# Optimization experiments

Hardware: AMD Instinct MI355X
Metric: run time of the kernel (lower is better)

## Reference

```python
import jax, jax.numpy as jnp
import numpy as np

N_NODES = 100000
N_EDGES = 3200000
IN_CH = 64
HID = [64, 32, 16]


def setup_inputs() -> dict:
    key = jax.random.key(0)
    ks = jax.random.split(key, 12)
    x = jax.random.normal(ks[0], (N_NODES, IN_CH), dtype=jnp.float32)
    edge_index = jax.random.randint(ks[1], (2, N_EDGES), 0, N_NODES, dtype=jnp.int32)
    dims = [IN_CH] + HID
    params = {}
    i = 2
    for l in range(3):
        din, dout = dims[l], dims[l + 1]
        sc = 1.0 / np.sqrt(din)
        params[f"Wl{l}"] = jax.random.uniform(ks[i], (din, dout), jnp.float32, -sc, sc); i += 1
        params[f"Wr{l}"] = jax.random.uniform(ks[i], (din, dout), jnp.float32, -sc, sc); i += 1
        params[f"b{l}"] = jnp.zeros((dout,), jnp.float32)
    sc = 1.0 / np.sqrt(HID[-1])
    params["Wc"] = jax.random.uniform(ks[i], (HID[-1], 1), jnp.float32, -sc, sc)
    params["bc"] = jnp.zeros((1,), jnp.float32)
    return dict(x=x, edge_index=edge_index, **params)


def _sage_conv(x, src, dst, Wl, Wr, b):
    # message = x[src]; mean-aggregate at dst; out = agg @ Wl + x @ Wr + b
    msg = x[src]  # [E, din]
    s = jax.ops.segment_sum(msg, dst, num_segments=N_NODES)
    cnt = jax.ops.segment_sum(jnp.ones((dst.shape[0],), x.dtype), dst, num_segments=N_NODES)
    agg = s / jnp.maximum(cnt, 1.0)[:, None]
    return agg @ Wl + x @ Wr + b


def reference(x, edge_index, Wl0, Wr0, b0, Wl1, Wr1, b1, Wl2, Wr2, b2, Wc, bc):
    src, dst = edge_index[0], edge_index[1]
    h = jax.nn.relu(_sage_conv(x, src, dst, Wl0, Wr0, b0))
    h = jax.nn.relu(_sage_conv(h, src, dst, Wl1, Wr1, b1))
    h = jax.nn.relu(_sage_conv(h, src, dst, Wl2, Wr2, b2))
    return h @ Wc + bc  # [N_NODES, 1]
```

## Files before the change

### kernel.cpp

```cpp
#include <hip/hip_runtime.h>


#define NN 100000
#define BSH 6
#define NBK ((NN + 63) >> 6)
#define HB 128
#define SRCMASK 0x1FFFF
#define NSEG 8192
#define SCB 32

__device__ __forceinline__ unsigned f2bf(float f) {
    unsigned u = __float_as_uint(f);
    u += 0x7fffu + ((u >> 16) & 1u);
    return u >> 16;
}
__device__ __forceinline__ float bflo(unsigned u) { return __uint_as_float(u << 16); }
__device__ __forceinline__ float bfhi(unsigned u) { return __uint_as_float(u & 0xffff0000u); }

__global__ void hist_k(const int* __restrict__ dst, int E, int* __restrict__ gh) {
    __shared__ int lh[NBK];
    for (int i = threadIdx.x; i < NBK; i += blockDim.x) lh[i] = 0;
    __syncthreads();
    int c = blockIdx.x;
    int chunk = (E + HB - 1) / HB;
    int b0 = c * chunk, e0 = min(b0 + chunk, E);
    for (int e = b0 + threadIdx.x; e < e0; e += blockDim.x)
        atomicAdd(&lh[dst[e] >> BSH], 1);
    __syncthreads();
    for (int i = threadIdx.x; i < NBK; i += blockDim.x) gh[i * HB + c] = lh[i];
}

__global__ void scanA_k(const int* __restrict__ gh, int M, int* __restrict__ segsum) {
    int t = blockIdx.x * blockDim.x + threadIdx.x;
    int cht = (M + NSEG - 1) / NSEG;
    int b0 = t * cht, e0 = min(b0 + cht, M);
    int s = 0;
    for (int i = b0; i < e0; ++i) s += gh[i];
    segsum[t] = s;
}

__global__ void scanB_k(int* __restrict__ segsum, int* __restrict__ gh, int M, int E) {
    __shared__ int part[1024];
    int tid = threadIdx.x;
    constexpr int SPT = NSEG / 1024;
    int loc[SPT];
    int s = 0;
#pragma unroll
    for (int k = 0; k < SPT; ++k) { loc[k] = segsum[tid * SPT + k]; s += loc[k]; }
    part[tid] = s;
    __syncthreads();
    for (int d = 1; d < 1024; d <<= 1) {
        int t = (tid >= d) ? part[tid - d] : 0;
        __syncthreads();
        part[tid] += t;
        __syncthreads();
    }
    int run = (tid == 0) ? 0 : part[tid - 1];
#pragma unroll
    for (int k = 0; k < SPT; ++k) { int t = loc[k]; segsum[tid * SPT + k] = run; run += t; }
    if (tid == 0) gh[M] = E;
}

__global__ void scanC_k(int* __restrict__ gh, int M, const int* __restrict__ segsum) {
    int t = blockIdx.x * blockDim.x + threadIdx.x;
    int cht = (M + NSEG - 1) / NSEG;
    int b0 = t * cht, e0 = min(b0 + cht, M);
    int run = segsum[t];
    for (int i = b0; i < e0; ++i) {
        int v = gh[i];
        gh[i] = run;
        run += v;
    }
}

__global__ void scatter_pack_k(const int* __restrict__ src, const int* __restrict__ dst,
                               int E, const int* __restrict__ gh,
                               unsigned* __restrict__ pair) {
    __shared__ int cur[NBK];
    int c = blockIdx.x;
    for (int i = threadIdx.x; i < NBK; i += blockDim.x) cur[i] = gh[i * HB + c];
    __syncthreads();
    int chunk = (E + HB - 1) / HB;
    int b0 = c * chunk, e0 = min(b0 + chunk, E);
    for (int e = b0 + threadIdx.x; e < e0; e += blockDim.x) {
        int dv = dst[e], sv = src[e];
        int p = atomicAdd(&cur[dv >> BSH], 1);
        pair[p] = (unsigned)sv | ((unsigned)(dv & 63) << 17);
    }
}

__global__ void sort_bucket_k(const unsigned* __restrict__ pair, const int* __restrict__ gh,
                              int* __restrict__ adj, int* __restrict__ off,
                              float* __restrict__ inv, int N, int E) {
    __shared__ int lcnt[64];
    __shared__ int lbase[64];
    int b = blockIdx.x, tid = threadIdx.x;
    int base = gh[b * HB], endp = gh[(b + 1) * HB];
    int v0 = b << BSH;
    int nv = min(64, N - v0);
    if (tid < 64) lcnt[tid] = 0;
    __syncthreads();
    for (int i = base + tid; i < endp; i += blockDim.x)
        atomicAdd(&lcnt[pair[i] >> 17], 1);
    __syncthreads();
    if (tid == 0) {
        int run = 0;
        for (int d = 0; d < 64; ++d) { lbase[d] = run; run += lcnt[d]; }
    }
    __syncthreads();
    if (tid < nv) {
        off[v0 + tid] = base + lbase[tid];
        inv[v0 + tid] = 1.0f / (float)max(lcnt[tid], 1);
    }
    if (b == NBK - 1 && tid == 0) off[N] = E;
    if (tid < 64) lcnt[tid] = lbase[tid];
    __syncthreads();
    for (int i = base + tid; i < endp; i += blockDim.x) {
        unsigned u = pair[i];
        int dl = u >> 17;
        int p = base + atomicAdd(&lcnt[dl], 1);
        adj[p] = u & SRCMASK;
    }
}

template <int DIN, int DOUT>
__global__ void transform2_k(const float* __restrict__ h,
                             const float* __restrict__ Wl, const float* __restrict__ Wr,
                             const float* __restrict__ bias,
                             unsigned* __restrict__ g, float2* __restrict__ r, int N) {
    constexpr int JP = DOUT / 2;
    __shared__ float2 sWl[DIN * JP];
    __shared__ float2 sWr[DIN * JP];
    __shared__ float2 sb[JP];
    const float2* Wl2 = (const float2*)Wl;
    const float2* Wr2 = (const float2*)Wr;
    for (int i = threadIdx.x; i < DIN * JP; i += blockDim.x) { sWl[i] = Wl2[i]; sWr[i] = Wr2[i]; }
    if (threadIdx.x < JP) sb[threadIdx.x] = ((const float2*)bias)[threadIdx.x];
    __syncthreads();
    int idx = blockIdx.x * blockDim.x + threadIdx.x;
    int NP = N / 2;
    if (idx >= NP * JP) return;
    int p = idx / JP, jp = idx % JP;
    int v0 = 2 * p, v1 = v0 + 1;
    const float* h0 = h + (size_t)v0 * DIN;
    const float* h1 = h + (size_t)v1 * DIN;
    float gl0x = 0, gl0y = 0, gl1x = 0, gl1y = 0;
    float gr0x = 0, gr0y = 0, gr1x = 0, gr1y = 0;
#pragma unroll
    for (int k = 0; k < DIN; ++k) {
        float2 wl = sWl[k * JP + jp];
        float2 wr = sWr[k * JP + jp];
        float a0 = h0[k], a1 = h1[k];
        gl0x = fmaf(a0, wl.x, gl0x); gl0y = fmaf(a0, wl.y, gl0y);
        gl1x = fmaf(a1, wl.x, gl1x); gl1y = fmaf(a1, wl.y, gl1y);
        gr0x = fmaf(a0, wr.x, gr0x); gr0y = fmaf(a0, wr.y, gr0y);
        gr1x = fmaf(a1, wr.x, gr1x); gr1y = fmaf(a1, wr.y, gr1y);
    }
    float2 bb = sb[jp];
    g[(size_t)v0 * JP + jp] = f2bf(gl0x) | (f2bf(gl0y) << 16);
    g[(size_t)v1 * JP + jp] = f2bf(gl1x) | (f2bf(gl1y) << 16);
    r[(size_t)v0 * JP + jp] = make_float2(gr0x + bb.x, gr0y + bb.y);
    r[(size_t)v1 * JP + jp] = make_float2(gr1x + bb.x, gr1y + bb.y);
}

template <int DOUT, int WAVES, int HEAD>
__global__ void agg_k(const unsigned* __restrict__ g, const int* __restrict__ off,
                      const int* __restrict__ adj, const float* __restrict__ invc,
                      const float* r, const float* __restrict__ Wc,
                      const float* __restrict__ bc, float* out, int N) {
    constexpr int Q8 = DOUT / 8;
    constexpr int EPT = 64 / Q8;
    __shared__ float sagg[WAVES][DOUT];
    int wid = threadIdx.x >> 6, lane = threadIdx.x & 63;
    int v = blockIdx.x * WAVES + wid;
    bool active = v < N;
    int q = lane & (Q8 - 1);
    int eg = lane / Q8;
    float acc[8] = {0, 0, 0, 0, 0, 0, 0, 0};
#define ACCU(U) do { \
        acc[0] += bflo(U.x); acc[1] += bfhi(U.x); \
        acc[2] += bflo(U.y); acc[3] += bfhi(U.y); \
        acc[4] += bflo(U.z); acc[5] += bfhi(U.z); \
        acc[6] += bflo(U.w); acc[7] += bfhi(U.w); } while (0)
    if (active) {
        int beg = off[v], end = off[v + 1];
        const uint4* g4 = (const uint4*)g;
        int i = beg + eg;
        for (; i + 3 * EPT < end; i += 4 * EPT) {
            int s0 = adj[i], s1 = adj[i + EPT], s2 = adj[i + 2 * EPT], s3 = adj[i + 3 * EPT];
            uint4 u0 = g4[(size_t)s0 * Q8 + q];
            uint4 u1 = g4[(size_t)s1 * Q8 + q];
            uint4 u2 = g4[(size_t)s2 * Q8 + q];
            uint4 u3 = g4[(size_t)s3 * Q8 + q];
            ACCU(u0); ACCU(u1); ACCU(u2); ACCU(u3);
        }
        for (; i < end; i += EPT) {
            int sv = adj[i];
            uint4 u = g4[(size_t)sv * Q8 + q];
            ACCU(u);
        }
#pragma unroll
        for (int d = Q8; d < 64; d <<= 1)
#pragma unroll
            for (int c = 0; c < 8; ++c) acc[c] += __shfl_xor(acc[c], d, 64);
        if (eg == 0) {
            float4* sp = (float4*)&sagg[wid][q * 8];
            sp[0] = make_float4(acc[0], acc[1], acc[2], acc[3]);
            sp[1] = make_float4(acc[4], acc[5], acc[6], acc[7]);
        }
    }
#undef ACCU
    __syncthreads();
    if (active && lane < DOUT) {
        float iv = invc[v];
        float val = fmaxf(fmaf(sagg[wid][lane], iv, r[(size_t)v * DOUT + lane]), 0.f);
        if (!HEAD) {
            out[(size_t)v * DOUT + lane] = val;
        } else {
            float pp = val * Wc[lane];
#pragma unroll
            for (int d = 1; d < 16; d <<= 1) pp += __shfl_xor(pp, d, 64);
            if (lane == 0) out[v] = pp + bc[0];
        }
    }
}

extern "C" void kernel_launch(void* const* d_in, const int* in_sizes, int n_in,
                              void* d_out, int out_size, void* d_ws, size_t ws_size,
                              hipStream_t stream) {
    const float* x   = (const float*)d_in[0];
    const int*   ei  = (const int*)d_in[1];
    const float* Wl0 = (const float*)d_in[2];
    const float* Wr0 = (const float*)d_in[3];
    const float* b0  = (const float*)d_in[4];
    const float* Wl1 = (const float*)d_in[5];
    const float* Wr1 = (const float*)d_in[6];
    const float* b1  = (const float*)d_in[7];
    const float* Wl2 = (const float*)d_in[8];
    const float* Wr2 = (const float*)d_in[9];
    const float* b2  = (const float*)d_in[10];
    const float* Wc  = (const float*)d_in[11];
    const float* bc  = (const float*)d_in[12];
    float* out = (float*)d_out;

    const int N = NN;
    const int E = in_sizes[1] / 2;
    const int* src = ei;
    const int* dst = ei + E;
    const int M = NBK * HB;

    char* ws = (char*)d_ws;
    const size_t KB = 1 << 10;
    const size_t MB = 1 << 20;
    int*      gh   = (int*)(ws + 0);
    int*      off  = (int*)(ws + 1 * MB);
    float*    inv  = (float*)(ws + 1536 * KB);
    int*      segs = (int*)(ws + 1950 * KB);
    unsigned* pair = (unsigned*)(ws + 2 * MB);
    int*      adj  = (int*)(ws + 15 * MB);
    unsigned* g0 = (unsigned*)(ws + 54 * MB);
    float*    r0 = (float*)(ws + 28 * MB);
    float*    h1 = r0;
    unsigned* g1 = (unsigned*)(ws + 2 * MB);
    float*    r1 = (float*)(ws + 54 * MB);
    float*    h2 = r1;
    unsigned* g2 = (unsigned*)(ws + 9 * MB);
    float*    r2 = (float*)(ws + 28 * MB);

    hist_k<<<HB, 256, 0, stream>>>(dst, E, gh);
    scanA_k<<<SCB, 256, 0, stream>>>(gh, M, segs);
    scanB_k<<<1, 1024, 0, stream>>>(segs, gh, M, E);
    scanC_k<<<SCB, 256, 0, stream>>>(gh, M, segs);
    scatter_pack_k<<<HB, 256, 0, stream>>>(src, dst, E, gh, pair);
    sort_bucket_k<<<NBK, 256, 0, stream>>>(pair, gh, adj, off, inv, N, E);

    transform2_k<64, 64><<<(N / 2 * 32 + 255) / 256, 256, 0, stream>>>(x, Wl0, Wr0, b0, g0, (float2*)r0, N);
    agg_k<64, 4, 0><<<(N + 3) / 4, 256, 0, stream>>>(g0, off, adj, inv, r0, nullptr, nullptr, h1, N);

    transform2_k<64, 32><<<(N / 2 * 16 + 255) / 256, 256, 0, stream>>>(h1, Wl1, Wr1, b1, g1, (float2*)r1, N);
    agg_k<32, 4, 0><<<(N + 3) / 4, 256, 0, stream>>>(g1, off, adj, inv, r1, nullptr, nullptr, h2, N);

    transform2_k<32, 16><<<(N / 2 * 8 + 255) / 256, 256, 0, stream>>>(h2, Wl2, Wr2, b2, g2, (float2*)r2, N);
    agg_k<16, 4, 1><<<(N + 3) / 4, 256, 0, stream>>>(g2, off, adj, inv, r2, Wc, bc, out, N);
}
```

Baseline: 442.2 us.

## Fuse histogram and local scatter into one pass, resolve bucket ranges per chunk

Replaces the separate histogram and global scatter kernels with a single kernel in which each of 256 chunks builds its local bucket histogram, does an in-block exclusive scan and scatters edges into its own contiguous region, keeping writes local to the chunk. A transpose kernel then reshapes the per-chunk counts and offsets so the global scan can run over them. The bucket sort kernel now reads each chunk's sub-range serially per thread instead of a single contiguous range. This removes the separate scatter pass over the edge list and its scattered global writes, but each sort thread now walks its segment serially and the bucket kernel's reads are split into many small pieces.

```diff
diff --git a/kernel.cpp b/kernel.cpp
--- a/kernel.cpp
+++ b/kernel.cpp
@@ -4,7 +4,7 @@
 #define NN 100000
 #define BSH 6
 #define NBK ((NN + 63) >> 6)
-#define HB 128
+#define HB 256
 #define SRCMASK 0x1FFFF
 #define NSEG 8192
 #define SCB 32
@@ -17,17 +17,74 @@
 __device__ __forceinline__ float bflo(unsigned u) { return __uint_as_float(u << 16); }
 __device__ __forceinline__ float bfhi(unsigned u) { return __uint_as_float(u & 0xffff0000u); }
 
-__global__ void hist_k(const int* __restrict__ dst, int E, int* __restrict__ gh) {
+__global__ void part1_k(const int* __restrict__ src, const int* __restrict__ dst,
+                        int E, int* __restrict__ ghT, int* __restrict__ gh2T,
+                        unsigned* __restrict__ pair) {
     __shared__ int lh[NBK];
-    for (int i = threadIdx.x; i < NBK; i += blockDim.x) lh[i] = 0;
-    __syncthreads();
-    int c = blockIdx.x;
+    __shared__ int part[512];
+    int c = blockIdx.x, tid = threadIdx.x;
     int chunk = (E + HB - 1) / HB;
     int b0 = c * chunk, e0 = min(b0 + chunk, E);
-    for (int e = b0 + threadIdx.x; e < e0; e += blockDim.x)
-        atomicAdd(&lh[dst[e] >> BSH], 1);
-    __syncthreads();
-    for (int i = threadIdx.x; i < NBK; i += blockDim.x) gh[i * HB + c] = lh[i];
+    for (int i = tid; i < NBK; i += 512) lh[i] = 0;
+    __syncthreads();
+    for (int e = b0 + tid; e < e0; e += 512) atomicAdd(&lh[dst[e] >> BSH], 1);
+    __syncthreads();
+    constexpr int CPT = (NBK + 511) / 512;
+    int myb = tid * CPT;
+    int s = 0;
+#pragma unroll
+    for (int k = 0; k < CPT; ++k) { int i = myb + k; if (i < NBK) s += lh[i]; }
+    part[tid] = s;
+    __syncthreads();
+    for (int d = 1; d < 512; d <<= 1) {
+        int t = (tid >= d) ? part[tid - d] : 0;
+        __syncthreads();
+        part[tid] += t;
+        __syncthreads();
+    }
+    int run = (tid == 0) ? 0 : part[tid - 1];
+#pragma unroll
+    for (int k = 0; k < CPT; ++k) {
+        int i = myb + k;
+        if (i < NBK) {
+            int cc = lh[i];
+            ghT[(size_t)c * NBK + i] = cc;
+            gh2T[(size_t)c * NBK + i] = run;
+            lh[i] = run;
+            run += cc;
+        }
+    }
+    __syncthreads();
+    for (int e = b0 + tid; e < e0; e += 512) {
+        int dv = dst[e], sv = src[e];
+        int p = b0 + atomicAdd(&lh[dv >> BSH], 1);
+        pair[p] = (unsigned)sv | ((unsigned)(dv & 63) << 17);
+    }
+}
+
+__global__ void transpose_k(const int* __restrict__ a, const int* __restrict__ b,
+                            int* __restrict__ at, int* __restrict__ bt) {
+    __shared__ int ta[32][33], tb[32][33];
+    int ib = blockIdx.x * 32;
+    int cb = blockIdx.y * 32;
+    int tx = threadIdx.x & 31, ty = threadIdx.x >> 5;
+#pragma unroll
+    for (int k = 0; k < 32; k += 8) {
+        int c = cb + ty + k, i = ib + tx;
+        if (c < HB && i < NBK) {
+            ta[ty + k][tx] = a[(size_t)c * NBK + i];
+            tb[ty + k][tx] = b[(size_t)c * NBK + i];
+        }
+    }
+    __syncthreads();
+#pragma unroll
+    for (int k = 0; k < 32; k += 8) {
+        int i = ib + ty + k, c = cb + tx;
+        if (i < NBK && c < HB) {
+            at[(size_t)i * HB + c] = ta[tx][ty + k];
+            bt[(size_t)i * HB + c] = tb[tx][ty + k];
+        }
+    }
 }
 
 __global__ void scanA_k(const int* __restrict__ gh, int M, int* __restrict__ segsum) {
@@ -39,7 +96,7 @@
     segsum[t] = s;
 }
 
-__global__ void scanB_k(int* __restrict__ segsum, int* __restrict__ gh, int M, int E) {
+__global__ void scanB_k(int* __restrict__ segsum) {
     __shared__ int part[1024];
     int tid = threadIdx.x;
     constexpr int SPT = NSEG / 1024;
@@ -58,7 +115,6 @@
     int run = (tid == 0) ? 0 : part[tid - 1];
 #pragma unroll
     for (int k = 0; k < SPT; ++k) { int t = loc[k]; segsum[tid * SPT + k] = run; run += t; }
-    if (tid == 0) gh[M] = E;
 }
 
 __global__ void scanC_k(int* __restrict__ gh, int M, const int* __restrict__ segsum) {
@@ -73,35 +129,24 @@
     }
 }
 
-__global__ void scatter_pack_k(const int* __restrict__ src, const int* __restrict__ dst,
-                               int E, const int* __restrict__ gh,
-                               unsigned* __restrict__ pair) {
-    __shared__ int cur[NBK];
-    int c = blockIdx.x;
-    for (int i = threadIdx.x; i < NBK; i += blockDim.x) cur[i] = gh[i * HB + c];
-    __syncthreads();
-    int chunk = (E + HB - 1) / HB;
-    int b0 = c * chunk, e0 = min(b0 + chunk, E);
-    for (int e = b0 + threadIdx.x; e < e0; e += blockDim.x) {
-        int dv = dst[e], sv = src[e];
-        int p = atomicAdd(&cur[dv >> BSH], 1);
-        pair[p] = (unsigned)sv | ((unsigned)(dv & 63) << 17);
-    }
-}
-
-__global__ void sort_bucket_k(const unsigned* __restrict__ pair, const int* __restrict__ gh,
+__global__ void sort_bucket_k(const unsigned* __restrict__ pair,
+                              const int* __restrict__ ghm, const int* __restrict__ gh2m,
                               int* __restrict__ adj, int* __restrict__ off,
                               float* __restrict__ inv, int N, int E) {
     __shared__ int lcnt[64];
     __shared__ int lbase[64];
     int b = blockIdx.x, tid = threadIdx.x;
-    int base = gh[b * HB], endp = gh[(b + 1) * HB];
+    int base = ghm[b * HB];
     int v0 = b << BSH;
     int nv = min(64, N - v0);
     if (tid < 64) lcnt[tid] = 0;
     __syncthreads();
-    for (int i = base + tid; i < endp; i += blockDim.x)
-        atomicAdd(&lcnt[pair[i] >> 17], 1);
+    int chunk = (E + HB - 1) / HB;
+    int c = tid;
+    int b0c = c * chunk, e0c = min(b0c + chunk, E);
+    int ls = b0c + gh2m[b * HB + c];
+    int le = (b == NBK - 1) ? e0c : (b0c + gh2m[(b + 1) * HB + c]);
+    for (int i = ls; i < le; ++i) atomicAdd(&lcnt[pair[i] >> 17], 1);
     __syncthreads();
     if (tid == 0) {
         int run = 0;
@@ -115,10 +160,9 @@
     if (b == NBK - 1 && tid == 0) off[N] = E;
     if (tid < 64) lcnt[tid] = lbase[tid];
     __syncthreads();
-    for (int i = base + tid; i < endp; i += blockDim.x) {
+    for (int i = ls; i < le; ++i) {
         unsigned u = pair[i];
-        int dl = u >> 17;
-        int p = base + atomicAdd(&lcnt[dl], 1);
+        int p = base + atomicAdd(&lcnt[u >> 17], 1);
         adj[p] = u & SRCMASK;
     }
 }
@@ -252,27 +296,30 @@
     char* ws = (char*)d_ws;
     const size_t KB = 1 << 10;
     const size_t MB = 1 << 20;
-    int*      gh   = (int*)(ws + 0);
-    int*      off  = (int*)(ws + 1 * MB);
-    float*    inv  = (float*)(ws + 1536 * KB);
-    int*      segs = (int*)(ws + 1950 * KB);
-    unsigned* pair = (unsigned*)(ws + 2 * MB);
-    int*      adj  = (int*)(ws + 15 * MB);
-    unsigned* g0 = (unsigned*)(ws + 54 * MB);
-    float*    r0 = (float*)(ws + 28 * MB);
+    int*      ghT  = (int*)(ws + 0);
+    int*      gh2T = (int*)(ws + 2 * MB);
+    int*      ghm  = (int*)(ws + 4 * MB);
+    int*      gh2m = (int*)(ws + 6 * MB);
+    int*      off  = (int*)(ws + 8 * MB);
+    float*    inv  = (float*)(ws + 8 * MB + 512 * KB);
+    int*      segs = (int*)(ws + 9 * MB);
+    unsigned* pair = (unsigned*)(ws + 10 * MB);
+    int*      adj  = (int*)(ws + 23 * MB);
+    unsigned* g0 = (unsigned*)(ws + 36 * MB);
+    float*    r0 = (float*)(ws + 49 * MB);
     float*    h1 = r0;
-    unsigned* g1 = (unsigned*)(ws + 2 * MB);
-    float*    r1 = (float*)(ws + 54 * MB);
+    unsigned* g1 = (unsigned*)(ws + 10 * MB);
+    float*    r1 = (float*)(ws + 36 * MB);
     float*    h2 = r1;
-    unsigned* g2 = (unsigned*)(ws + 9 * MB);
-    float*    r2 = (float*)(ws + 28 * MB);
-
-    hist_k<<<HB, 256, 0, stream>>>(dst, E, gh);
-    scanA_k<<<SCB, 256, 0, stream>>>(gh, M, segs);
-    scanB_k<<<1, 1024, 0, stream>>>(segs, gh, M, E);
-    scanC_k<<<SCB, 256, 0, stream>>>(gh, M, segs);
-    scatter_pack_k<<<HB, 256, 0, stream>>>(src, dst, E, gh, pair);
-    sort_bucket_k<<<NBK, 256, 0, stream>>>(pair, gh, adj, off, inv, N, E);
+    unsigned* g2 = (unsigned*)(ws + 17 * MB);
+    float*    r2 = (float*)(ws + 10 * MB);
+
+    part1_k<<<HB, 512, 0, stream>>>(src, dst, E, ghT, gh2T, pair);
+    transpose_k<<<dim3((NBK + 31) / 32, HB / 32), 256, 0, stream>>>(ghT, gh2T, ghm, gh2m);
+    scanA_k<<<SCB, 256, 0, stream>>>(ghm, M, segs);
+    scanB_k<<<1, 1024, 0, stream>>>(segs);
+    scanC_k<<<SCB, 256, 0, stream>>>(ghm, M, segs);
+    sort_bucket_k<<<NBK, HB, 0, stream>>>(pair, ghm, gh2m, adj, off, inv, N, E);
 
     transform2_k<64, 64><<<(N / 2 * 32 + 255) / 256, 256, 0, stream>>>(x, Wl0, Wr0, b0, g0, (float2*)r0, N);
     agg_k<64, 4, 0><<<(N + 3) / 4, 256, 0, stream>>>(g0, off, adj, inv, r0, nullptr, nullptr, h1, N);
```

Result: slower. 491.5 us (+11.2%).

## Restructure CSR build into three-kernel local-partition and bucket sort

Applied to the files above, without the earlier changes.

Replaces the six-kernel CSR construction (histogram, three-pass scan, scatter, per-64-node bucket sort) with three kernels. Each of 256 chunks histograms its edges into 196 coarse buckets of 512 nodes and scatters them locally within the chunk. A single block computes the bucket bases, and one block per bucket then gathers its slices from every chunk to produce the final adjacency lists, offsets and inverse degrees. This cuts launches and global scan passes, but the final sort walks each chunk slice serially per thread and runs only 196 blocks of 256 threads, which may underuse the GPU.

```diff
diff --git a/kernel.cpp b/kernel.cpp
--- a/kernel.cpp
+++ b/kernel.cpp
@@ -2,12 +2,11 @@
 
 
 #define NN 100000
-#define BSH 6
-#define NBK ((NN + 63) >> 6)
-#define HB 128
+#define BSH 9
+#define NBK ((NN + 511) >> 9)
+#define HB 256
 #define SRCMASK 0x1FFFF
-#define NSEG 8192
-#define SCB 32
+#define DLSH 17
 
 __device__ __forceinline__ unsigned f2bf(float f) {
     unsigned u = __float_as_uint(f);
@@ -17,108 +16,97 @@
 __device__ __forceinline__ float bflo(unsigned u) { return __uint_as_float(u << 16); }
 __device__ __forceinline__ float bfhi(unsigned u) { return __uint_as_float(u & 0xffff0000u); }
 
-__global__ void hist_k(const int* __restrict__ dst, int E, int* __restrict__ gh) {
+__global__ void part1_k(const int* __restrict__ src, const int* __restrict__ dst,
+                        int E, int* __restrict__ gcnt, int* __restrict__ goff,
+                        unsigned* __restrict__ pair) {
     __shared__ int lh[NBK];
-    for (int i = threadIdx.x; i < NBK; i += blockDim.x) lh[i] = 0;
-    __syncthreads();
-    int c = blockIdx.x;
+    __shared__ int part[512];
+    int c = blockIdx.x, tid = threadIdx.x;
     int chunk = (E + HB - 1) / HB;
     int b0 = c * chunk, e0 = min(b0 + chunk, E);
-    for (int e = b0 + threadIdx.x; e < e0; e += blockDim.x)
-        atomicAdd(&lh[dst[e] >> BSH], 1);
-    __syncthreads();
-    for (int i = threadIdx.x; i < NBK; i += blockDim.x) gh[i * HB + c] = lh[i];
-}
-
-__global__ void scanA_k(const int* __restrict__ gh, int M, int* __restrict__ segsum) {
-    int t = blockIdx.x * blockDim.x + threadIdx.x;
-    int cht = (M + NSEG - 1) / NSEG;
-    int b0 = t * cht, e0 = min(b0 + cht, M);
+    if (tid < NBK) lh[tid] = 0;
+    __syncthreads();
+    for (int e = b0 + tid; e < e0; e += 512) atomicAdd(&lh[dst[e] >> BSH], 1);
+    __syncthreads();
+    int cnt = (tid < NBK) ? lh[tid] : 0;
+    part[tid] = cnt;
+    __syncthreads();
+    for (int d = 1; d < 512; d <<= 1) {
+        int t = (tid >= d) ? part[tid - d] : 0;
+        __syncthreads();
+        part[tid] += t;
+        __syncthreads();
+    }
+    int run = (tid == 0) ? 0 : part[tid - 1];
+    if (tid < NBK) {
+        gcnt[(size_t)c * NBK + tid] = cnt;
+        goff[(size_t)c * NBK + tid] = run;
+        lh[tid] = run;
+    }
+    __syncthreads();
+    for (int e = b0 + tid; e < e0; e += 512) {
+        int dv = dst[e], sv = src[e];
+        int p = b0 + atomicAdd(&lh[dv >> BSH], 1);
+        pair[p] = (unsigned)sv | ((unsigned)(dv & 511) << DLSH);
+    }
+}
+
+__global__ void bsum_k(const int* __restrict__ gcnt, int* __restrict__ bb, int E) {
+    __shared__ int part[256];
+    int tid = threadIdx.x;
     int s = 0;
-    for (int i = b0; i < e0; ++i) s += gh[i];
-    segsum[t] = s;
-}
-
-__global__ void scanB_k(int* __restrict__ segsum, int* __restrict__ gh, int M, int E) {
-    __shared__ int part[1024];
-    int tid = threadIdx.x;
-    constexpr int SPT = NSEG / 1024;
-    int loc[SPT];
-    int s = 0;
-#pragma unroll
-    for (int k = 0; k < SPT; ++k) { loc[k] = segsum[tid * SPT + k]; s += loc[k]; }
+    if (tid < NBK)
+        for (int c = 0; c < HB; ++c) s += gcnt[(size_t)c * NBK + tid];
     part[tid] = s;
     __syncthreads();
-    for (int d = 1; d < 1024; d <<= 1) {
+    for (int d = 1; d < 256; d <<= 1) {
         int t = (tid >= d) ? part[tid - d] : 0;
         __syncthreads();
         part[tid] += t;
         __syncthreads();
     }
+    if (tid < NBK) bb[tid] = part[tid] - s;
+    if (tid == 0) bb[NBK] = E;
+}
+
+__global__ void sort2_k(const unsigned* __restrict__ pair, const int* __restrict__ goff,
+                        const int* __restrict__ bb, int* __restrict__ adj,
+                        int* __restrict__ off, float* __restrict__ inv, int N, int E) {
+    __shared__ int sls[HB], sle[HB];
+    __shared__ int lcnt[512], lcur[512];
+    __shared__ int part[256];
+    int b = blockIdx.x, tid = threadIdx.x;
+    int chunk = (E + HB - 1) / HB;
+    int b0c = tid * chunk, e0c = min(b0c + chunk, E);
+    sls[tid] = b0c + goff[(size_t)tid * NBK + b];
+    sle[tid] = (b + 1 < NBK) ? (b0c + goff[(size_t)tid * NBK + b + 1]) : e0c;
+    lcnt[tid] = 0; lcnt[tid + 256] = 0;
+    __syncthreads();
+    for (int i = sls[tid]; i < sle[tid]; ++i)
+        atomicAdd(&lcnt[pair[i] >> DLSH], 1);
+    __syncthreads();
+    int c0 = lcnt[2 * tid], c1 = lcnt[2 * tid + 1];
+    part[tid] = c0 + c1;
+    __syncthreads();
+    for (int d = 1; d < 256; d <<= 1) {
+        int t = (tid >= d) ? part[tid - d] : 0;
+        __syncthreads();
+        part[tid] += t;
+        __syncthreads();
+    }
     int run = (tid == 0) ? 0 : part[tid - 1];
-#pragma unroll
-    for (int k = 0; k < SPT; ++k) { int t = loc[k]; segsum[tid * SPT + k] = run; run += t; }
-    if (tid == 0) gh[M] = E;
-}
-
-__global__ void scanC_k(int* __restrict__ gh, int M, const int* __restrict__ segsum) {
-    int t = blockIdx.x * blockDim.x + threadIdx.x;
-    int cht = (M + NSEG - 1) / NSEG;
-    int b0 = t * cht, e0 = min(b0 + cht, M);
-    int run = segsum[t];
-    for (int i = b0; i < e0; ++i) {
-        int v = gh[i];
-        gh[i] = run;
-        run += v;
-    }
-}
-
-__global__ void scatter_pack_k(const int* __restrict__ src, const int* __restrict__ dst,
-                               int E, const int* __restrict__ gh,
-                               unsigned* __restrict__ pair) {
-    __shared__ int cur[NBK];
-    int c = blockIdx.x;
-    for (int i = threadIdx.x; i < NBK; i += blockDim.x) cur[i] = gh[i * HB + c];
-    __syncthreads();
-    int chunk = (E + HB - 1) / HB;
-    int b0 = c * chunk, e0 = min(b0 + chunk, E);
-    for (int e = b0 + threadIdx.x; e < e0; e += blockDim.x) {
-        int dv = dst[e], sv = src[e];
-        int p = atomicAdd(&cur[dv >> BSH], 1);
-        pair[p] = (unsigned)sv | ((unsigned)(dv & 63) << 17);
-    }
-}
-
-__global__ void sort_bucket_k(const unsigned* __restrict__ pair, const int* __restrict__ gh,
-                              int* __restrict__ adj, int* __restrict__ off,
-                              float* __restrict__ inv, int N, int E) {
-    __shared__ int lcnt[64];
-    __shared__ int lbase[64];
-    int b = blockIdx.x, tid = threadIdx.x;
-    int base = gh[b * HB], endp = gh[(b + 1) * HB];
+    int base = bb[b];
     int v0 = b << BSH;
-    int nv = min(64, N - v0);
-    if (tid < 64) lcnt[tid] = 0;
-    __syncthreads();
-    for (int i = base + tid; i < endp; i += blockDim.x)
-        atomicAdd(&lcnt[pair[i] >> 17], 1);
-    __syncthreads();
-    if (tid == 0) {
-        int run = 0;
-        for (int d = 0; d < 64; ++d) { lbase[d] = run; run += lcnt[d]; }
-    }
-    __syncthreads();
-    if (tid < nv) {
-        off[v0 + tid] = base + lbase[tid];
-        inv[v0 + tid] = 1.0f / (float)max(lcnt[tid], 1);
-    }
+    int vg0 = v0 + 2 * tid, vg1 = v0 + 2 * tid + 1;
+    if (vg0 < N) { off[vg0] = base + run;      inv[vg0] = 1.f / (float)max(c0, 1); }
+    if (vg1 < N) { off[vg1] = base + run + c0; inv[vg1] = 1.f / (float)max(c1, 1); }
+    lcur[2 * tid] = base + run;
+    lcur[2 * tid + 1] = base + run + c0;
     if (b == NBK - 1 && tid == 0) off[N] = E;
-    if (tid < 64) lcnt[tid] = lbase[tid];
-    __syncthreads();
-    for (int i = base + tid; i < endp; i += blockDim.x) {
+    __syncthreads();
+    for (int i = sls[tid]; i < sle[tid]; ++i) {
         unsigned u = pair[i];
-        int dl = u >> 17;
-        int p = base + atomicAdd(&lcnt[dl], 1);
+        int p = atomicAdd(&lcur[u >> DLSH], 1);
         adj[p] = u & SRCMASK;
     }
 }
@@ -247,32 +235,28 @@
     const int E = in_sizes[1] / 2;
     const int* src = ei;
     const int* dst = ei + E;
-    const int M = NBK * HB;
 
     char* ws = (char*)d_ws;
-    const size_t KB = 1 << 10;
     const size_t MB = 1 << 20;
-    int*      gh   = (int*)(ws + 0);
-    int*      off  = (int*)(ws + 1 * MB);
-    float*    inv  = (float*)(ws + 1536 * KB);
-    int*      segs = (int*)(ws + 1950 * KB);
-    unsigned* pair = (unsigned*)(ws + 2 * MB);
-    int*      adj  = (int*)(ws + 15 * MB);
-    unsigned* g0 = (unsigned*)(ws + 54 * MB);
-    float*    r0 = (float*)(ws + 28 * MB);
+    int*      gcnt = (int*)(ws + 0);
+    int*      goff = (int*)(ws + 1 * MB);
+    int*      bb   = (int*)(ws + 2 * MB);
+    int*      off  = (int*)(ws + 3 * MB);
+    float*    inv  = (float*)(ws + 3 * MB + 512 * 1024);
+    unsigned* pair = (unsigned*)(ws + 4 * MB);
+    int*      adj  = (int*)(ws + 17 * MB);
+    unsigned* g0 = (unsigned*)(ws + 30 * MB);
+    float*    r0 = (float*)(ws + 43 * MB);
     float*    h1 = r0;
-    unsigned* g1 = (unsigned*)(ws + 2 * MB);
-    float*    r1 = (float*)(ws + 54 * MB);
+    unsigned* g1 = (unsigned*)(ws + 4 * MB);
+    float*    r1 = (float*)(ws + 30 * MB);
     float*    h2 = r1;
-    unsigned* g2 = (unsigned*)(ws + 9 * MB);
-    float*    r2 = (float*)(ws + 28 * MB);
-
-    hist_k<<<HB, 256, 0, stream>>>(dst, E, gh);
-    scanA_k<<<SCB, 256, 0, stream>>>(gh, M, segs);
-    scanB_k<<<1, 1024, 0, stream>>>(segs, gh, M, E);
-    scanC_k<<<SCB, 256, 0, stream>>>(gh, M, segs);
-    scatter_pack_k<<<HB, 256, 0, stream>>>(src, dst, E, gh, pair);
-    sort_bucket_k<<<NBK, 256, 0, stream>>>(pair, gh, adj, off, inv, N, E);
+    unsigned* g2 = (unsigned*)(ws + 11 * MB);
+    float*    r2 = (float*)(ws + 43 * MB);
+
+    part1_k<<<HB, 512, 0, stream>>>(src, dst, E, gcnt, goff, pair);
+    bsum_k<<<1, 256, 0, stream>>>(gcnt, bb, E);
+    sort2_k<<<NBK, HB, 0, stream>>>(pair, goff, bb, adj, off, inv, N, E);
 
     transform2_k<64, 64><<<(N / 2 * 32 + 255) / 256, 256, 0, stream>>>(x, Wl0, Wr0, b0, g0, (float2*)r0, N);
     agg_k<64, 4, 0><<<(N + 3) / 4, 256, 0, stream>>>(g0, off, adj, inv, r0, nullptr, nullptr, h1, N);
```

Measured after the change: 434.3 us. No clear change (-1.8%).
